# Kernel optimization log

Hardware: AMD Instinct MI355X
Metric: run time of the kernel (lower is better)

The kernel has to match this reference:

```python
import math
import jax, jax.numpy as jnp
import numpy as np

N_ANGLES = 8
RADIUS_WIDTH = 8
OVERLAP_RATIO = 1.5
EPS = 1e-8


def _build_masks(H, W):
    # radius bin index [H,W] and normalized overlapping angular soft weights [A,H,W]
    cy, cx = H // 2, W // 2
    y, x = jnp.meshgrid(jnp.arange(H, dtype=jnp.float32), jnp.arange(W, dtype=jnp.float32), indexing='ij')
    dy, dx = y - cy, x - cx
    r = jnp.sqrt(dy ** 2 + dx ** 2)
    theta = (jnp.arctan2(dy, dx) + math.pi) % math.pi
    n_radii = int(max(cy, cx) // RADIUS_WIDTH) + 1
    radius_idx = jnp.clip(jnp.floor(r / RADIUS_WIDTH).astype(jnp.int32), 0, n_radii - 1)
    delta = math.pi / N_ANGLES
    half_width = OVERLAP_RATIO * delta / 2.0
    centers = (jnp.arange(N_ANGLES, dtype=jnp.float32) + 0.5) * delta  # [A]
    dist = jnp.abs(theta[None, :, :] - centers[:, None, None])        # [A,H,W]
    w = jnp.clip(1.0 - dist / half_width, 0.0, None) * (dist < half_width).astype(jnp.float32)
    angle_weights = w / (w.sum(axis=0, keepdims=True) + EPS)          # [A,H,W]
    return radius_idx, angle_weights, n_radii


def setup_inputs() -> dict:
    key = jax.random.key(0)
    k1, k2, k3, k4 = jax.random.split(key, 4)
    B, C, H, W = 8, 256, 128, 128
    c_mid = 16
    n_radii = (max(H // 2, W // 2) // RADIUS_WIDTH) + 1  # = 9
    x = jax.random.normal(k1, (B, C, H, W), dtype=jnp.float32)
    w_in = jax.random.normal(k2, (c_mid, C), dtype=jnp.float32) * 0.05   # 1x1 conv proj_in
    w_out = jax.random.normal(k3, (C, c_mid), dtype=jnp.float32) * 0.05  # 1x1 conv proj_out
    freq_weights = 1.0 + 0.1 * jax.random.normal(k4, (c_mid, N_ANGLES, n_radii), dtype=jnp.float32)
    return {"x": x, "w_in": w_in, "w_out": w_out, "freq_weights": freq_weights}


def reference(x, w_in, w_out, freq_weights):
    B, C, H, W = x.shape
    radius_idx, angle_weights, n_radii = _build_masks(H, W)
    # 1x1 conv in
    x_proj = jnp.einsum('bchw,mc->bmhw', x, w_in)                      # [B,c_mid,H,W]
    # FFT -> centered spectrum
    x_fft = jnp.fft.fftshift(jnp.fft.fft2(x_proj, norm='ortho'), axes=(-2, -1))
    mag = jnp.abs(x_fft) + EPS
    theta = jnp.angle(x_fft)
    # gain[c,h,w] = sum_a angle_weights[a,h,w] * freq_weights[c, a, radius_idx[h,w]]
    w_sel = freq_weights[:, :, radius_idx]                             # [c_mid,A,H,W] gather
    gain = jnp.einsum('ahw,cahw->chw', angle_weights, w_sel)           # [c_mid,H,W]
    mag_enh = mag * gain[None]                                         # [B,c_mid,H,W]
    x_fft_enh = mag_enh * jnp.exp(1j * theta)
    x_enh = jnp.fft.ifft2(jnp.fft.ifftshift(x_fft_enh, axes=(-2, -1)), norm='ortho').real
    out = x + jnp.einsum('bmhw,cm->bchw', x_enh, w_out)                # residual + 1x1 conv out
    return out
```

## Files before the change

### kernel.cpp

```cpp
#include <hip/hip_runtime.h>
#include <math.h>

#define NB   8
#define CIN  256
#define CMID 16
#define NH   128
#define NW   128
#define HWSZ 16384
#define HW4  4096
#define NANG 8
#define NRAD 9

typedef float    f32x4_t __attribute__((ext_vector_type(4)));
typedef unsigned u32x2_t __attribute__((ext_vector_type(2)));

__device__ __forceinline__ unsigned short f2bf(float f) {
    unsigned u = __float_as_uint(f);
    u += 0x7fffu + ((u >> 16) & 1u);
    return (unsigned short)(u >> 16);
}
__device__ __forceinline__ float bf_lo(unsigned u) { return __uint_as_float(u << 16); }
__device__ __forceinline__ float bf_hi(unsigned u) { return __uint_as_float(u & 0xffff0000u); }
__device__ __forceinline__ unsigned pack2(float a, float b) {
    return (unsigned)f2bf(a) | ((unsigned)f2bf(b) << 16);
}

__device__ __forceinline__ int bitrev7(int v) {
    return (int)(__brev((unsigned)v) >> 25);
}

__global__ void __launch_bounds__(256) gain_kernel(const float* __restrict__ fw,
                                                   float* __restrict__ gain) {
    int p  = blockIdx.x * 256 + threadIdx.x;
    int py = p >> 7, px = p & 127;
    int fy = bitrev7(py), fx = bitrev7(px);
    int hy = (fy + 64) & 127, hx = (fx + 64) & 127;
    float dy = (float)(hy - 64), dx = (float)(hx - 64);
    float r = sqrtf(dy * dy + dx * dx);
    int ridx = (int)floorf(r * 0.125f);
    if (ridx > NRAD - 1) ridx = NRAD - 1;
    const float PI_F = 3.14159265358979323846f;
    float theta = fmodf(atan2f(dy, dx) + PI_F, PI_F);
    const float delta = (float)(M_PI / 8.0);
    const float hwid  = (float)(1.5 * (M_PI / 8.0) / 2.0);
    float wv[NANG];
    float wsum = 0.f;
#pragma unroll
    for (int a = 0; a < NANG; ++a) {
        float c = ((float)a + 0.5f) * delta;
        float dist = fabsf(theta - c);
        float wa = fmaxf(1.0f - dist / hwid, 0.0f);
        if (!(dist < hwid)) wa = 0.0f;
        wv[a] = wa;
        wsum += wa;
    }
    float inv = 1.0f / (wsum + 1e-8f);
#pragma unroll
    for (int m = 0; m < CMID; ++m) {
        float g = 0.f;
#pragma unroll
        for (int a = 0; a < NANG; ++a)
            g += wv[a] * fw[(m * NANG + a) * NRAD + ridx];
        gain[m * HWSZ + p] = g * inv * (1.0f / 16384.0f);
    }
}

__global__ void __launch_bounds__(256, 4) proj_partial(const float* __restrict__ x,
                                                       const float* __restrict__ w_in,
                                                       unsigned short* __restrict__ partials,
                                                       int nchunk) {
    int b  = blockIdx.z;
    int ck = blockIdx.y;
    int p4 = blockIdx.x * 256 + threadIdx.x;
    int cpc = CIN / nchunk;
    int c0 = ck * cpc;
    const f32x4_t* xb = (const f32x4_t*)(x + (size_t)b * CIN * HWSZ);
    f32x4_t acc[CMID];
#pragma unroll
    for (int m = 0; m < CMID; ++m) acc[m] = (f32x4_t){0.f, 0.f, 0.f, 0.f};
    for (int c = c0; c < c0 + cpc; c += 8) {
        f32x4_t v[8];
#pragma unroll
        for (int k = 0; k < 8; ++k)
            v[k] = xb[(size_t)(c + k) * HW4 + p4];
#pragma unroll
        for (int k = 0; k < 8; ++k) {
#pragma unroll
            for (int m = 0; m < CMID; ++m)
                acc[m] += w_in[m * CIN + c + k] * v[k];
        }
    }
    ushort4* pb = (ushort4*)partials + ((size_t)(b * nchunk + ck) * CMID) * HW4;
#pragma unroll
    for (int m = 0; m < CMID; ++m)
        pb[(size_t)m * HW4 + p4] = make_ushort4(f2bf(acc[m].x), f2bf(acc[m].y),
                                                f2bf(acc[m].z), f2bf(acc[m].w));
}

__global__ void __launch_bounds__(256) reduce_fft_rows(const unsigned short* __restrict__ partials,
                                                       unsigned* __restrict__ xf,
                                                       int nchunk) {
    __shared__ float2 lds[512];
    int img = blockIdx.y;
    int b = img >> 4, m = img & 15;
    int r0 = blockIdx.x * 4;
    int t = threadIdx.x;
    const unsigned* pbase = (const unsigned*)(partials +
        ((size_t)(b * nchunk) * CMID + m) * HWSZ + (size_t)r0 * NW) + t;
    size_t cks = (size_t)CMID * HWSZ / 2;
    float sx = 0.f, sy = 0.f;
    if (nchunk == 8) {
#pragma unroll
        for (int ck = 0; ck < 8; ++ck) {
            unsigned u = pbase[(size_t)ck * cks];
            sx += bf_lo(u); sy += bf_hi(u);
        }
    } else {
        for (int ck = 0; ck < nchunk; ++ck) {
            unsigned u = pbase[(size_t)ck * cks];
            sx += bf_lo(u); sy += bf_hi(u);
        }
    }
    lds[2 * t]     = make_float2(sx, 0.f);
    lds[2 * t + 1] = make_float2(sy, 0.f);
    __syncthreads();
    const float PI_F = 3.14159265358979323846f;
    int j = t & 63;
    float2* row = lds + (t >> 6) * 128;
    for (int ls = 6; ls >= 0; --ls) {
        int s = 1 << ls;
        int off = j & (s - 1);
        int i0 = ((j >> ls) << (ls + 1)) + off;
        float ang = -PI_F * (float)off / (float)s;
        float sn, cs;
        __sincosf(ang, &sn, &cs);
        float2 a = row[i0];
        float2 bb = row[i0 + s];
        row[i0] = make_float2(a.x + bb.x, a.y + bb.y);
        float dx_ = a.x - bb.x, dy_ = a.y - bb.y;
        row[i0 + s] = make_float2(dx_ * cs - dy_ * sn, dx_ * sn + dy_ * cs);
        __syncthreads();
    }
    unsigned* xo = xf + (size_t)img * HWSZ + (size_t)r0 * NW;
#pragma unroll
    for (int ii = 0; ii < 2; ++ii) {
        int px = ii * 256 + t;
        xo[px] = pack2(lds[px].x, lds[px].y);
    }
}

__global__ void __launch_bounds__(256) fft_cols_gain(unsigned* __restrict__ xf,
                                                     const float* __restrict__ gain) {
    __shared__ float2 buf[128 * 33];
    int img = blockIdx.y;
    int m   = img & (CMID - 1);
    int c0  = blockIdx.x * 32;
    int t   = threadIdx.x;
    unsigned* xi = xf + (size_t)img * HWSZ;

    for (int idx = t; idx < 128 * 32; idx += 256) {
        int r = idx >> 5, lc = idx & 31;
        unsigned u = xi[r * NW + c0 + lc];
        buf[r * 33 + lc] = make_float2(bf_lo(u), bf_hi(u));
    }
    __syncthreads();
    const float PI_F = 3.14159265358979323846f;
    int lc = t & 31;
    int jb = t >> 5;
    for (int ls = 6; ls >= 0; --ls) {
        int s = 1 << ls;
        for (int j = jb; j < 64; j += 8) {
            int off = j & (s - 1);
            int i0 = ((j >> ls) << (ls + 1)) + off;
            float ang = -PI_F * (float)off / (float)s;
            float sn, cs;
            __sincosf(ang, &sn, &cs);
            float2 a = buf[i0 * 33 + lc];
            float2 bb = buf[(i0 + s) * 33 + lc];
            buf[i0 * 33 + lc] = make_float2(a.x + bb.x, a.y + bb.y);
            float dx_ = a.x - bb.x, dy_ = a.y - bb.y;
            buf[(i0 + s) * 33 + lc] = make_float2(dx_ * cs - dy_ * sn, dx_ * sn + dy_ * cs);
        }
        __syncthreads();
    }
    {
        const float* gm = gain + (size_t)m * HWSZ;
        for (int idx = t; idx < 128 * 32; idx += 256) {
            int r = idx >> 5, lcc = idx & 31;
            float g = gm[r * NW + c0 + lcc];
            buf[r * 33 + lcc].x *= g;
            buf[r * 33 + lcc].y *= g;
        }
        __syncthreads();
    }
    for (int ls = 0; ls <= 6; ++ls) {
        int s = 1 << ls;
        for (int j = jb; j < 64; j += 8) {
            int off = j & (s - 1);
            int i0 = ((j >> ls) << (ls + 1)) + off;
            float ang = PI_F * (float)off / (float)s;
            float sn, cs;
            __sincosf(ang, &sn, &cs);
            float2 a = buf[i0 * 33 + lc];
            float2 bb = buf[(i0 + s) * 33 + lc];
            float tx = bb.x * cs - bb.y * sn, ty = bb.x * sn + bb.y * cs;
            buf[i0 * 33 + lc] = make_float2(a.x + tx, a.y + ty);
            buf[(i0 + s) * 33 + lc] = make_float2(a.x - tx, a.y - ty);
        }
        __syncthreads();
    }
    for (int idx = t; idx < 128 * 32; idx += 256) {
        int r = idx >> 5, lcc = idx & 31;
        xi[r * NW + c0 + lcc] = pack2(buf[r * 33 + lcc].x, buf[r * 33 + lcc].y);
    }
}

__global__ void __launch_bounds__(256) ifft_rows(const unsigned* __restrict__ xf,
                                                 unsigned short* __restrict__ xe) {
    __shared__ float2 lds[512];
    int img = blockIdx.y;
    int r0 = blockIdx.x * 4;
    int t = threadIdx.x;
    const unsigned* xi = xf + (size_t)img * HWSZ + (size_t)r0 * NW;
#pragma unroll
    for (int ii = 0; ii < 2; ++ii) {
        int px = ii * 256 + t;
        unsigned u = xi[px];
        lds[px] = make_float2(bf_lo(u), bf_hi(u));
    }
    __syncthreads();
    const float PI_F = 3.14159265358979323846f;
    int j = t & 63;
    float2* row = lds + (t >> 6) * 128;
    for (int ls = 0; ls <= 6; ++ls) {
        int s = 1 << ls;
        int off = j & (s - 1);
        int i0 = ((j >> ls) << (ls + 1)) + off;
        float ang = PI_F * (float)off / (float)s;
        float sn, cs;
        __sincosf(ang, &sn, &cs);
        float2 a = row[i0];
        float2 bb = row[i0 + s];
        float tx = bb.x * cs - bb.y * sn, ty = bb.x * sn + bb.y * cs;
        row[i0] = make_float2(a.x + tx, a.y + ty);
        row[i0 + s] = make_float2(a.x - tx, a.y - ty);
        __syncthreads();
    }
    unsigned* xo = (unsigned*)xe + (((size_t)img * HWSZ + (size_t)r0 * NW) >> 1) + t;
    xo[0] = pack2(lds[2 * t].x, lds[2 * t + 1].x);
}

__global__ void __launch_bounds__(256, 4) out_kernel(const float* __restrict__ x,
                                                     const float* __restrict__ w_out,
                                                     const unsigned short* __restrict__ xe,
                                                     float* __restrict__ out) {
    int b  = blockIdx.z;
    int ct = blockIdx.y;
    int p4 = blockIdx.x * 256 + threadIdx.x;
    const u32x2_t* xeb = (const u32x2_t*)(xe + (size_t)b * CMID * HWSZ);
    f32x4_t e[CMID];
#pragma unroll
    for (int m = 0; m < CMID; ++m) {
        u32x2_t u = xeb[(size_t)m * HW4 + p4];
        e[m] = (f32x4_t){ bf_lo(u.x), bf_hi(u.x), bf_lo(u.y), bf_hi(u.y) };
    }
    const f32x4_t* xb = (const f32x4_t*)(x + (size_t)b * CIN * HWSZ);
    f32x4_t* ob = (f32x4_t*)(out + (size_t)b * CIN * HWSZ);
    int c0 = ct * 16;
    for (int c = c0; c < c0 + 16; c += 4) {
        f32x4_t a0 = xb[(size_t)(c + 0) * HW4 + p4];
        f32x4_t a1 = xb[(size_t)(c + 1) * HW4 + p4];
        f32x4_t a2 = xb[(size_t)(c + 2) * HW4 + p4];
        f32x4_t a3 = xb[(size_t)(c + 3) * HW4 + p4];
#pragma unroll
        for (int m = 0; m < CMID; ++m) {
            a0 += w_out[(c + 0) * CMID + m] * e[m];
            a1 += w_out[(c + 1) * CMID + m] * e[m];
            a2 += w_out[(c + 2) * CMID + m] * e[m];
            a3 += w_out[(c + 3) * CMID + m] * e[m];
        }
        __builtin_nontemporal_store(a0, ob + (size_t)(c + 0) * HW4 + p4);
        __builtin_nontemporal_store(a1, ob + (size_t)(c + 1) * HW4 + p4);
        __builtin_nontemporal_store(a2, ob + (size_t)(c + 2) * HW4 + p4);
        __builtin_nontemporal_store(a3, ob + (size_t)(c + 3) * HW4 + p4);
    }
}

extern "C" void kernel_launch(void* const* d_in, const int* in_sizes, int n_in,
                              void* d_out, int out_size, void* d_ws, size_t ws_size,
                              hipStream_t stream) {
    const float* x     = (const float*)d_in[0];
    const float* w_in  = (const float*)d_in[1];
    const float* w_out = (const float*)d_in[2];
    const float* fw    = (const float*)d_in[3];
    float* out = (float*)d_out;

    int nchunk = 8;
    while (nchunk > 1) {
        size_t need = (size_t)NB * nchunk * CMID * HWSZ * 2
                    + (size_t)NB * CMID * HWSZ * 4
                    + (size_t)CMID * HWSZ * 4;
        if (need <= ws_size) break;
        nchunk >>= 1;
    }
    unsigned short* partials = (unsigned short*)d_ws;
    unsigned* xfu = (unsigned*)(partials + (size_t)NB * nchunk * CMID * HWSZ);
    float*    gain = (float*)(xfu + (size_t)NB * CMID * HWSZ);
    unsigned short* xe = partials;

    gain_kernel<<<HWSZ / 256, 256, 0, stream>>>(fw, gain);
    proj_partial<<<dim3(HW4 / 256, nchunk, NB), 256, 0, stream>>>(x, w_in, partials, nchunk);
    reduce_fft_rows<<<dim3(NH / 4, NB * CMID), 256, 0, stream>>>(partials, xfu, nchunk);
    fft_cols_gain<<<dim3(NW / 32, NB * CMID), 256, 0, stream>>>(xfu, gain);
    ifft_rows<<<dim3(NH / 4, NB * CMID), 256, 0, stream>>>(xfu, xe);
    out_kernel<<<dim3(HW4 / 256, CIN / 16, NB), 256, 0, stream>>>(x, w_out, xe, out);
}
```

Measured before the change: 116.5 us.

## Fuse inverse row FFT with output projection and residual into one kernel

Merges the row iFFT and the 1x1 output convolution into a single kernel. Each block loads two spectrum rows for all 16 mid channels into LDS, runs the iFFT, writes a bf16 real result back to LDS, then applies w_out and the residual for all 256 channels. The real-output trick merges the final butterfly stage and keeps only real parts. This removes the bf16 x_enh round trip through global memory and one kernel launch. In exchange there are only 512 blocks with heavier per-thread work (32 output channels each), so latency hiding over the large x/out streams may suffer.

```diff
diff --git a/kernel.cpp b/kernel.cpp
--- a/kernel.cpp
+++ b/kernel.cpp
@@ -13,6 +13,7 @@
 
 typedef float    f32x4_t __attribute__((ext_vector_type(4)));
 typedef unsigned u32x2_t __attribute__((ext_vector_type(2)));
+typedef unsigned u32x4_t __attribute__((ext_vector_type(4)));
 
 __device__ __forceinline__ unsigned short f2bf(float f) {
     unsigned u = __float_as_uint(f);
@@ -215,74 +216,90 @@
     }
 }
 
-__global__ void __launch_bounds__(256) ifft_rows(const unsigned* __restrict__ xf,
-                                                 unsigned short* __restrict__ xe) {
-    __shared__ float2 lds[512];
-    int img = blockIdx.y;
-    int r0 = blockIdx.x * 4;
-    int t = threadIdx.x;
-    const unsigned* xi = xf + (size_t)img * HWSZ + (size_t)r0 * NW;
-#pragma unroll
-    for (int ii = 0; ii < 2; ++ii) {
-        int px = ii * 256 + t;
-        unsigned u = xi[px];
-        lds[px] = make_float2(bf_lo(u), bf_hi(u));
+__global__ void __launch_bounds__(512, 4) ifft_out(const unsigned* __restrict__ xf,
+                                                   const float* __restrict__ x,
+                                                   const float* __restrict__ w_out,
+                                                   float* __restrict__ out) {
+    __shared__ float2 img[CMID * 256];
+    __shared__ unsigned short ebf[CMID * 256];
+    int b  = blockIdx.y;
+    int r0 = blockIdx.x * 2;
+    int t  = threadIdx.x;
+    {
+        int m = t >> 5, q2 = t & 31;
+        const unsigned* src = xf + ((size_t)(b * CMID + m)) * HWSZ + (size_t)r0 * NW + q2 * 8;
+#pragma unroll
+        for (int h = 0; h < 2; ++h) {
+            u32x4_t u = *(const u32x4_t*)(src + h * 4);
+#pragma unroll
+            for (int k = 0; k < 4; ++k)
+                img[m * 256 + q2 * 8 + h * 4 + k] = make_float2(bf_lo(u[k]), bf_hi(u[k]));
+        }
     }
     __syncthreads();
     const float PI_F = 3.14159265358979323846f;
-    int j = t & 63;
-    float2* row = lds + (t >> 6) * 128;
-    for (int ls = 0; ls <= 6; ++ls) {
+    int j = t & 63, f0 = t >> 6;
+    for (int ls = 0; ls <= 5; ++ls) {
         int s = 1 << ls;
         int off = j & (s - 1);
         int i0 = ((j >> ls) << (ls + 1)) + off;
         float ang = PI_F * (float)off / (float)s;
         float sn, cs;
         __sincosf(ang, &sn, &cs);
-        float2 a = row[i0];
-        float2 bb = row[i0 + s];
-        float tx = bb.x * cs - bb.y * sn, ty = bb.x * sn + bb.y * cs;
-        row[i0] = make_float2(a.x + tx, a.y + ty);
-        row[i0 + s] = make_float2(a.x - tx, a.y - ty);
-        __syncthreads();
-    }
-    unsigned* xo = (unsigned*)xe + (((size_t)img * HWSZ + (size_t)r0 * NW) >> 1) + t;
-    xo[0] = pack2(lds[2 * t].x, lds[2 * t + 1].x);
-}
-
-__global__ void __launch_bounds__(256, 4) out_kernel(const float* __restrict__ x,
-                                                     const float* __restrict__ w_out,
-                                                     const unsigned short* __restrict__ xe,
-                                                     float* __restrict__ out) {
-    int b  = blockIdx.z;
-    int ct = blockIdx.y;
-    int p4 = blockIdx.x * 256 + threadIdx.x;
-    const u32x2_t* xeb = (const u32x2_t*)(xe + (size_t)b * CMID * HWSZ);
-    f32x4_t e[CMID];
-#pragma unroll
-    for (int m = 0; m < CMID; ++m) {
-        u32x2_t u = xeb[(size_t)m * HW4 + p4];
-        e[m] = (f32x4_t){ bf_lo(u.x), bf_hi(u.x), bf_lo(u.y), bf_hi(u.y) };
-    }
-    const f32x4_t* xb = (const f32x4_t*)(x + (size_t)b * CIN * HWSZ);
-    f32x4_t* ob = (f32x4_t*)(out + (size_t)b * CIN * HWSZ);
-    int c0 = ct * 16;
-    for (int c = c0; c < c0 + 16; c += 4) {
-        f32x4_t a0 = xb[(size_t)(c + 0) * HW4 + p4];
-        f32x4_t a1 = xb[(size_t)(c + 1) * HW4 + p4];
-        f32x4_t a2 = xb[(size_t)(c + 2) * HW4 + p4];
-        f32x4_t a3 = xb[(size_t)(c + 3) * HW4 + p4];
+#pragma unroll
+        for (int ff = 0; ff < 4; ++ff) {
+            int f = f0 + ff * 8;
+            float2* row = img + (f >> 1) * 256 + (f & 1) * 128;
+            float2 a = row[i0];
+            float2 bb = row[i0 + s];
+            float tx = bb.x * cs - bb.y * sn, ty = bb.x * sn + bb.y * cs;
+            row[i0] = make_float2(a.x + tx, a.y + ty);
+            row[i0 + s] = make_float2(a.x - tx, a.y - ty);
+        }
+        __syncthreads();
+    }
+    {
+        float ang = PI_F * (float)j * (1.0f / 64.0f);
+        float sn, cs;
+        __sincosf(ang, &sn, &cs);
+#pragma unroll
+        for (int ff = 0; ff < 4; ++ff) {
+            int f = f0 + ff * 8;
+            int base = (f >> 1) * 256 + (f & 1) * 128;
+            float2 a = img[base + j];
+            float2 bb = img[base + j + 64];
+            float tx = bb.x * cs - bb.y * sn;
+            ebf[base + j]      = f2bf(a.x + tx);
+            ebf[base + j + 64] = f2bf(a.x - tx);
+        }
+    }
+    __syncthreads();
+    int p4 = t & 63, cg = t >> 6;
+    u32x2_t ep[CMID];
+    const u32x2_t* eb = (const u32x2_t*)ebf;
+#pragma unroll
+    for (int m = 0; m < CMID; ++m) ep[m] = eb[m * 64 + p4];
+    const f32x4_t* xb = (const f32x4_t*)(x + (size_t)b * CIN * HWSZ) + (size_t)r0 * 32 + p4;
+    f32x4_t* ob = (f32x4_t*)(out + (size_t)b * CIN * HWSZ) + (size_t)r0 * 32 + p4;
+    int c0 = cg * 32;
+    for (int c = c0; c < c0 + 32; c += 4) {
+        f32x4_t a0 = xb[(size_t)(c + 0) * HW4];
+        f32x4_t a1 = xb[(size_t)(c + 1) * HW4];
+        f32x4_t a2 = xb[(size_t)(c + 2) * HW4];
+        f32x4_t a3 = xb[(size_t)(c + 3) * HW4];
 #pragma unroll
         for (int m = 0; m < CMID; ++m) {
-            a0 += w_out[(c + 0) * CMID + m] * e[m];
-            a1 += w_out[(c + 1) * CMID + m] * e[m];
-            a2 += w_out[(c + 2) * CMID + m] * e[m];
-            a3 += w_out[(c + 3) * CMID + m] * e[m];
-        }
-        __builtin_nontemporal_store(a0, ob + (size_t)(c + 0) * HW4 + p4);
-        __builtin_nontemporal_store(a1, ob + (size_t)(c + 1) * HW4 + p4);
-        __builtin_nontemporal_store(a2, ob + (size_t)(c + 2) * HW4 + p4);
-        __builtin_nontemporal_store(a3, ob + (size_t)(c + 3) * HW4 + p4);
+            f32x4_t e = (f32x4_t){ bf_lo(ep[m].x), bf_hi(ep[m].x),
+                                   bf_lo(ep[m].y), bf_hi(ep[m].y) };
+            a0 += w_out[(c + 0) * CMID + m] * e;
+            a1 += w_out[(c + 1) * CMID + m] * e;
+            a2 += w_out[(c + 2) * CMID + m] * e;
+            a3 += w_out[(c + 3) * CMID + m] * e;
+        }
+        __builtin_nontemporal_store(a0, ob + (size_t)(c + 0) * HW4);
+        __builtin_nontemporal_store(a1, ob + (size_t)(c + 1) * HW4);
+        __builtin_nontemporal_store(a2, ob + (size_t)(c + 2) * HW4);
+        __builtin_nontemporal_store(a3, ob + (size_t)(c + 3) * HW4);
     }
 }
 
@@ -306,12 +323,10 @@
     unsigned short* partials = (unsigned short*)d_ws;
     unsigned* xfu = (unsigned*)(partials + (size_t)NB * nchunk * CMID * HWSZ);
     float*    gain = (float*)(xfu + (size_t)NB * CMID * HWSZ);
-    unsigned short* xe = partials;
 
     gain_kernel<<<HWSZ / 256, 256, 0, stream>>>(fw, gain);
     proj_partial<<<dim3(HW4 / 256, nchunk, NB), 256, 0, stream>>>(x, w_in, partials, nchunk);
     reduce_fft_rows<<<dim3(NH / 4, NB * CMID), 256, 0, stream>>>(partials, xfu, nchunk);
     fft_cols_gain<<<dim3(NW / 32, NB * CMID), 256, 0, stream>>>(xfu, gain);
-    ifft_rows<<<dim3(NH / 4, NB * CMID), 256, 0, stream>>>(xfu, xe);
-    out_kernel<<<dim3(HW4 / 256, CIN / 16, NB), 256, 0, stream>>>(x, w_out, xe, out);
-}
+    ifft_out<<<dim3(NH / 2, NB), 512, 0, stream>>>(xfu, x, w_out, out);
+}
```

Result: slower. 144.0 us (+23.6%).

## Fuse channel projection with row FFT, reducing partials in LDS

Applied to the files above, without the earlier changes.

Replaces the chunked projection kernel, which wrote bf16 partial sums to global memory, and the separate reduce-plus-row-FFT kernel with a single kernel. Each block handles a two-row strip for all 16 mid channels, splits input channels across 8 waves, reduces them in shared memory and runs the row FFTs in place. This removes the partials round-trip through global memory and one launch, at the cost of fewer, larger blocks and bf16 rounding in the intra-block reduction.

```diff
diff --git a/kernel.cpp b/kernel.cpp
--- a/kernel.cpp
+++ b/kernel.cpp
@@ -23,6 +23,15 @@
 __device__ __forceinline__ float bf_hi(unsigned u) { return __uint_as_float(u & 0xffff0000u); }
 __device__ __forceinline__ unsigned pack2(float a, float b) {
     return (unsigned)f2bf(a) | ((unsigned)f2bf(b) << 16);
+}
+__device__ __forceinline__ ushort4 pack4(f32x4_t v) {
+    return make_ushort4(f2bf(v.x), f2bf(v.y), f2bf(v.z), f2bf(v.w));
+}
+__device__ __forceinline__ f32x4_t unpack4(ushort4 u) {
+    return (f32x4_t){ __uint_as_float((unsigned)u.x << 16),
+                      __uint_as_float((unsigned)u.y << 16),
+                      __uint_as_float((unsigned)u.z << 16),
+                      __uint_as_float((unsigned)u.w << 16) };
 }
 
 __device__ __forceinline__ int bitrev7(int v) {
@@ -65,68 +74,65 @@
     }
 }
 
-__global__ void __launch_bounds__(256, 4) proj_partial(const float* __restrict__ x,
-                                                       const float* __restrict__ w_in,
-                                                       unsigned short* __restrict__ partials,
-                                                       int nchunk) {
-    int b  = blockIdx.z;
-    int ck = blockIdx.y;
-    int p4 = blockIdx.x * 256 + threadIdx.x;
-    int cpc = CIN / nchunk;
-    int c0 = ck * cpc;
-    const f32x4_t* xb = (const f32x4_t*)(x + (size_t)b * CIN * HWSZ);
-    f32x4_t acc[CMID];
-#pragma unroll
-    for (int m = 0; m < CMID; ++m) acc[m] = (f32x4_t){0.f, 0.f, 0.f, 0.f};
-    for (int c = c0; c < c0 + cpc; c += 8) {
+__global__ void __launch_bounds__(512, 4) proj_fft(const float* __restrict__ x,
+                                                   const float* __restrict__ w_in,
+                                                   unsigned* __restrict__ xf) {
+    __shared__ ushort4 red[CMID][4][64];
+    float2* fftbuf = (float2*)red;
+    int b = blockIdx.y, strip = blockIdx.x;
+    int t = threadIdx.x;
+    int w = t >> 6, l = t & 63;
+
+    const f32x4_t* xb = (const f32x4_t*)(x + (size_t)b * CIN * HWSZ) + strip * 64 + l;
+    f32x4_t facc[CMID];
+#pragma unroll
+    for (int m = 0; m < CMID; ++m) facc[m] = (f32x4_t){0.f, 0.f, 0.f, 0.f};
+    int c0 = w * 32;
+    for (int c = c0; c < c0 + 32; c += 8) {
         f32x4_t v[8];
 #pragma unroll
         for (int k = 0; k < 8; ++k)
-            v[k] = xb[(size_t)(c + k) * HW4 + p4];
+            v[k] = xb[(size_t)(c + k) * HW4];
 #pragma unroll
         for (int k = 0; k < 8; ++k) {
 #pragma unroll
             for (int m = 0; m < CMID; ++m)
-                acc[m] += w_in[m * CIN + c + k] * v[k];
-        }
-    }
-    ushort4* pb = (ushort4*)partials + ((size_t)(b * nchunk + ck) * CMID) * HW4;
-#pragma unroll
-    for (int m = 0; m < CMID; ++m)
-        pb[(size_t)m * HW4 + p4] = make_ushort4(f2bf(acc[m].x), f2bf(acc[m].y),
-                                                f2bf(acc[m].z), f2bf(acc[m].w));
-}
-
-__global__ void __launch_bounds__(256) reduce_fft_rows(const unsigned short* __restrict__ partials,
-                                                       unsigned* __restrict__ xf,
-                                                       int nchunk) {
-    __shared__ float2 lds[512];
-    int img = blockIdx.y;
-    int b = img >> 4, m = img & 15;
-    int r0 = blockIdx.x * 4;
-    int t = threadIdx.x;
-    const unsigned* pbase = (const unsigned*)(partials +
-        ((size_t)(b * nchunk) * CMID + m) * HWSZ + (size_t)r0 * NW) + t;
-    size_t cks = (size_t)CMID * HWSZ / 2;
-    float sx = 0.f, sy = 0.f;
-    if (nchunk == 8) {
-#pragma unroll
-        for (int ck = 0; ck < 8; ++ck) {
-            unsigned u = pbase[(size_t)ck * cks];
-            sx += bf_lo(u); sy += bf_hi(u);
-        }
-    } else {
-        for (int ck = 0; ck < nchunk; ++ck) {
-            unsigned u = pbase[(size_t)ck * cks];
-            sx += bf_lo(u); sy += bf_hi(u);
-        }
-    }
-    lds[2 * t]     = make_float2(sx, 0.f);
-    lds[2 * t + 1] = make_float2(sy, 0.f);
+                facc[m] += w_in[m * CIN + c + k] * v[k];
+        }
+    }
+    if (w >= 4) {
+#pragma unroll
+        for (int m = 0; m < CMID; ++m) red[m][w - 4][l] = pack4(facc[m]);
+    }
+    __syncthreads();
+    if (w < 4) {
+#pragma unroll
+        for (int m = 0; m < CMID; ++m) {
+            facc[m] += unpack4(red[m][w][l]);
+            red[m][w][l] = pack4(facc[m]);
+        }
+    }
+    __syncthreads();
+    ushort4 c4[2][4];
+#pragma unroll
+    for (int mm = 0; mm < 2; ++mm)
+#pragma unroll
+        for (int k = 0; k < 4; ++k)
+            c4[mm][k] = red[2 * w + mm][k][l];
+    __syncthreads();
+#pragma unroll
+    for (int mm = 0; mm < 2; ++mm) {
+        int m = 2 * w + mm;
+        f32x4_t s = unpack4(c4[mm][0]) + unpack4(c4[mm][1]) +
+                    unpack4(c4[mm][2]) + unpack4(c4[mm][3]);
+        fftbuf[m * 256 + 4 * l + 0] = make_float2(s.x, 0.f);
+        fftbuf[m * 256 + 4 * l + 1] = make_float2(s.y, 0.f);
+        fftbuf[m * 256 + 4 * l + 2] = make_float2(s.z, 0.f);
+        fftbuf[m * 256 + 4 * l + 3] = make_float2(s.w, 0.f);
+    }
     __syncthreads();
     const float PI_F = 3.14159265358979323846f;
-    int j = t & 63;
-    float2* row = lds + (t >> 6) * 128;
+    int j = l;
     for (int ls = 6; ls >= 0; --ls) {
         int s = 1 << ls;
         int off = j & (s - 1);
@@ -134,18 +140,20 @@
         float ang = -PI_F * (float)off / (float)s;
         float sn, cs;
         __sincosf(ang, &sn, &cs);
-        float2 a = row[i0];
-        float2 bb = row[i0 + s];
-        row[i0] = make_float2(a.x + bb.x, a.y + bb.y);
-        float dx_ = a.x - bb.x, dy_ = a.y - bb.y;
-        row[i0 + s] = make_float2(dx_ * cs - dy_ * sn, dx_ * sn + dy_ * cs);
-        __syncthreads();
-    }
-    unsigned* xo = xf + (size_t)img * HWSZ + (size_t)r0 * NW;
-#pragma unroll
-    for (int ii = 0; ii < 2; ++ii) {
-        int px = ii * 256 + t;
-        xo[px] = pack2(lds[px].x, lds[px].y);
+        for (int f = w; f < 32; f += 8) {
+            float2* row = fftbuf + f * 128;
+            float2 a = row[i0];
+            float2 bb = row[i0 + s];
+            row[i0] = make_float2(a.x + bb.x, a.y + bb.y);
+            float dx_ = a.x - bb.x, dy_ = a.y - bb.y;
+            row[i0 + s] = make_float2(dx_ * cs - dy_ * sn, dx_ * sn + dy_ * cs);
+        }
+        __syncthreads();
+    }
+    unsigned* xo = xf + (size_t)(b * CMID) * HWSZ + strip * 256;
+    for (int i = t; i < CMID * 256; i += 512) {
+        int m = i >> 8, px = i & 255;
+        xo[(size_t)m * HWSZ + px] = pack2(fftbuf[i].x, fftbuf[i].y);
     }
 }
 
@@ -295,22 +303,12 @@
     const float* fw    = (const float*)d_in[3];
     float* out = (float*)d_out;
 
-    int nchunk = 8;
-    while (nchunk > 1) {
-        size_t need = (size_t)NB * nchunk * CMID * HWSZ * 2
-                    + (size_t)NB * CMID * HWSZ * 4
-                    + (size_t)CMID * HWSZ * 4;
-        if (need <= ws_size) break;
-        nchunk >>= 1;
-    }
-    unsigned short* partials = (unsigned short*)d_ws;
-    unsigned* xfu = (unsigned*)(partials + (size_t)NB * nchunk * CMID * HWSZ);
+    unsigned* xfu = (unsigned*)d_ws;
     float*    gain = (float*)(xfu + (size_t)NB * CMID * HWSZ);
-    unsigned short* xe = partials;
+    unsigned short* xe = (unsigned short*)(gain + (size_t)CMID * HWSZ);
 
     gain_kernel<<<HWSZ / 256, 256, 0, stream>>>(fw, gain);
-    proj_partial<<<dim3(HW4 / 256, nchunk, NB), 256, 0, stream>>>(x, w_in, partials, nchunk);
-    reduce_fft_rows<<<dim3(NH / 4, NB * CMID), 256, 0, stream>>>(partials, xfu, nchunk);
+    proj_fft<<<dim3(64, NB), 512, 0, stream>>>(x, w_in, xfu);
     fft_cols_gain<<<dim3(NW / 32, NB * CMID), 256, 0, stream>>>(xfu, gain);
     ifft_rows<<<dim3(NH / 4, NB * CMID), 256, 0, stream>>>(xfu, xe);
     out_kernel<<<dim3(HW4 / 256, CIN / 16, NB), 256, 0, stream>>>(x, w_out, xe, out);
```

Result: slower. 183.9 us (+57.9%).
